# Optimization experiments

Hardware: AMD Instinct MI355X
Metric: run time of the kernel (lower is better)

The kernel has to match this reference:

```python
import jax, jax.numpy as jnp
import numpy as np

# ---- config (mirrors init_kwargs) ----
D_MODEL = 1024
D_STATE = 128
EXPAND = 2
HEADDIM = 64
D_INNER = D_MODEL * EXPAND            # 2048
NHEADS = D_INNER // HEADDIM           # 32
ROPE_FRACTION = 0.5
ROTATE_DIM = (int(D_STATE * ROPE_FRACTION) // 2) * 2   # 64
NUM_ANGLES = ROTATE_DIM // 2          # 32
A_FLOOR = 1e-4
EPS = 1e-5
IN_PROJ_DIM = 2 * D_INNER + 2 * D_STATE + 3 * NHEADS + NUM_ANGLES  # 4480
BATCH, SEQLEN = 2, 2048


def _state_rmsnorm(x, w):
    rms = jnp.sqrt(jnp.mean(x * x, axis=-1, keepdims=True) + EPS)
    return x / rms * w


def _apply_rotary_pairs(x, phase):
    # x: (b,s,h,d_state), phase: (b,s,h,num_pairs)
    if ROTATE_DIM == 0:
        return x
    x_rot = x[..., :ROTATE_DIM].reshape(*x.shape[:-1], ROTATE_DIM // 2, 2)
    x_pass = x[..., ROTATE_DIM:]
    cos = jnp.cos(phase)
    sin = jnp.sin(phase)
    real = x_rot[..., 0]
    imag = x_rot[..., 1]
    rr = real * cos - imag * sin
    ri = real * sin + imag * cos
    rotated = jnp.stack([rr, ri], axis=-1).reshape(*x.shape[:-1], ROTATE_DIM)
    if x_pass.shape[-1] == 0:
        return rotated
    return jnp.concatenate([rotated, x_pass], axis=-1)


def setup_inputs() -> dict:
    key = jax.random.key(0)
    ks = jax.random.split(key, 5)
    x = jax.random.normal(ks[0], (BATCH, SEQLEN, D_MODEL), jnp.float32)
    W_in = jax.random.normal(ks[1], (IN_PROJ_DIM, D_MODEL), jnp.float32) / np.sqrt(D_MODEL)
    # dt_bias ~ inverse-softplus of dt sampled in [dt_min, dt_max]
    dt = jnp.exp(jax.random.uniform(ks[2], (NHEADS,), jnp.float32) * (np.log(0.1) - np.log(0.001)) + np.log(0.001))
    dt = jnp.clip(dt, 1e-4)
    dt_bias = dt + jnp.log(-jnp.expm1(-dt))
    B_norm_w = jnp.ones((D_STATE,), jnp.float32)
    C_norm_w = jnp.ones((D_STATE,), jnp.float32)
    B_bias = jnp.ones((NHEADS, D_STATE), jnp.float32)
    C_bias = jnp.ones((NHEADS, D_STATE), jnp.float32)
    D_param = jnp.ones((NHEADS,), jnp.float32)
    out_norm_w = jnp.ones((D_INNER,), jnp.float32)
    W_out = jax.random.normal(ks[3], (D_MODEL, D_INNER), jnp.float32) / np.sqrt(D_INNER)
    return {"x": x, "W_in": W_in, "dt_bias": dt_bias, "B_norm_w": B_norm_w,
            "C_norm_w": C_norm_w, "B_bias": B_bias, "C_bias": C_bias,
            "D_param": D_param, "out_norm_w": out_norm_w, "W_out": W_out}


def reference(x, W_in, dt_bias, B_norm_w, C_norm_w, B_bias, C_bias, D_param, out_norm_w, W_out):
    b, s, _ = x.shape
    proj = jnp.einsum('bsd,pd->bsp', x, W_in)
    sizes = [D_INNER, D_INNER, D_STATE, D_STATE, NHEADS, NHEADS, NHEADS, NUM_ANGLES]
    offs = np.cumsum([0] + sizes)
    z, v, B_raw, C_raw, dd_dt, dd_A, trap_logits, angle_logits = [
        proj[..., offs[i]:offs[i + 1]] for i in range(8)]
    z = z.reshape(b, s, NHEADS, HEADDIM)
    v = v.reshape(b, s, NHEADS, HEADDIM)
    Bm = _state_rmsnorm(B_raw, B_norm_w)[:, :, None, :] + B_bias[None, None]   # (b,s,h,n)
    Cm = _state_rmsnorm(C_raw, C_norm_w)[:, :, None, :] + C_bias[None, None]
    dt = jax.nn.softplus(dd_dt + dt_bias[None, None])          # (b,s,h)
    A = jnp.minimum(-jax.nn.softplus(dd_A), -A_FLOOR)          # (b,s,h)
    trap = jax.nn.sigmoid(trap_logits)                          # (b,s,h)
    phase = jnp.cumsum(angle_logits, axis=1)[:, :, None, :]     # (b,s,1,angles)
    phase = jnp.broadcast_to(phase, (b, s, NHEADS, NUM_ANGLES))
    Bm = _apply_rotary_pairs(Bm, phase)
    Cm = _apply_rotary_pairs(Cm, phase)

    alpha = jnp.exp(A * dt)               # (b,s,h)
    beta = (1.0 - trap) * dt * alpha
    gamma = trap * dt

    # move time to leading for scan: (s, b, h, ...)
    def tl(a):
        return jnp.moveaxis(a, 1, 0)
    xs = (tl(alpha), tl(beta), tl(gamma), tl(Bm), tl(Cm), tl(v))

    state0 = jnp.zeros((b, NHEADS, HEADDIM, D_STATE), jnp.float32)
    pk0 = jnp.zeros((b, NHEADS, D_STATE), jnp.float32)
    pv0 = jnp.zeros((b, NHEADS, HEADDIM), jnp.float32)

    def step(carry, inp):
        state, pk, pv = carry
        a_t, b_t, g_t, k_t, q_t, v_t = inp
        prev_outer = pv[..., :, None] * pk[..., None, :]        # (b,h,p,n)
        curr_outer = v_t[..., :, None] * k_t[..., None, :]
        state = (a_t[..., None, None] * state
                 + b_t[..., None, None] * prev_outer
                 + g_t[..., None, None] * curr_outer)
        y_t = jnp.einsum('bhpn,bhn->bhp', state, q_t) + D_param[None, :, None] * v_t
        return (state, k_t, v_t), y_t

    _, ys = jax.lax.scan(step, (state0, pk0, pv0), xs)
    y = jnp.moveaxis(ys, 0, 1).reshape(b, s, D_INNER)
    z = z.reshape(b, s, D_INNER)
    # GatedRMSNorm
    rms = jnp.sqrt(jnp.mean(y * y, axis=-1, keepdims=True) + EPS)
    y = (y / rms * out_norm_w) * jax.nn.silu(z)
    return jnp.einsum('bsi,di->bsd', y, W_out)
```

## Files before the change

kernel.cpp:

```cpp
#include <hip/hip_runtime.h>
#include <math.h>

#define S_LEN 2048
#define NBATCH 2
#define DMODEL 1024
#define PDIM 4480
#define DI 2048
#define NH 32
#define HD 64
#define DS 128
#define NA 32
#define CHK 64
#define NC (S_LEN / CHK)
#define OFF_Z 0
#define OFF_V 2048
#define OFF_B 4096
#define OFF_C 4224
#define OFF_DT 4352
#define OFF_A 4384
#define OFF_TRAP 4416
#define OFF_ANG 4448

typedef __attribute__((ext_vector_type(8))) short s8v;
typedef __attribute__((ext_vector_type(4))) float f4v;

__device__ __forceinline__ float softplus_f(float x) {
    return x > 20.f ? x : log1pf(expf(x));
}

__device__ __forceinline__ ushort f2bf(float f) {
    unsigned u = __float_as_uint(f);
    unsigned r = (u + 0x7fffu + ((u >> 16) & 1u)) >> 16;
    return (ushort)r;
}

__device__ __forceinline__ uint4 pack8(const float* f) {
    uint4 o;
    o.x = (unsigned)f2bf(f[0]) | ((unsigned)f2bf(f[1]) << 16);
    o.y = (unsigned)f2bf(f[2]) | ((unsigned)f2bf(f[3]) << 16);
    o.z = (unsigned)f2bf(f[4]) | ((unsigned)f2bf(f[5]) << 16);
    o.w = (unsigned)f2bf(f[6]) | ((unsigned)f2bf(f[7]) << 16);
    return o;
}

__device__ __forceinline__ float bf2f(ushort u) {
    return __uint_as_float(((unsigned)u) << 16);
}
__device__ __forceinline__ float bf_lo(unsigned u) { return __uint_as_float(u << 16); }
__device__ __forceinline__ float bf_hi(unsigned u) { return __uint_as_float(u & 0xffff0000u); }

#define NCX  524288
#define NCWI 573440
#define NCWO 262144
__global__ __launch_bounds__(256)
void f2bf_all(const float* __restrict__ x, const float* __restrict__ wi,
              const float* __restrict__ wo, ushort* __restrict__ xbf,
              ushort* __restrict__ wibf, ushort* __restrict__ wobf) {
    int idx = blockIdx.x * 256 + threadIdx.x;
    const float* src; ushort* dst; int shift, rel;
    if (idx < NCX)              { rel = idx;               src = x;  dst = xbf;  shift = 7; }
    else if (idx < NCX + NCWI)  { rel = idx - NCX;         src = wi; dst = wibf; shift = 7; }
    else                        { rel = idx - NCX - NCWI;  src = wo; dst = wobf; shift = 8; }
    int dc = rel ^ ((rel >> shift) & 7);
    const float* ip = src + (size_t)rel * 8;
    float4 v0 = *(const float4*)ip;
    float4 v1 = *(const float4*)(ip + 4);
    uint4 o;
    o.x = (unsigned)f2bf(v0.x) | ((unsigned)f2bf(v0.y) << 16);
    o.y = (unsigned)f2bf(v0.z) | ((unsigned)f2bf(v0.w) << 16);
    o.z = (unsigned)f2bf(v1.x) | ((unsigned)f2bf(v1.y) << 16);
    o.w = (unsigned)f2bf(v1.z) | ((unsigned)f2bf(v1.w) << 16);
    *(uint4*)(dst + (size_t)dc * 8) = o;
}

__global__ __launch_bounds__(256, 2)
void gemm_bf16(const ushort* __restrict__ A, const ushort* __restrict__ B,
               float* __restrict__ C, int M, int N, int K) {
    __shared__ __align__(16) short lA[128 * 64];
    __shared__ __align__(16) short lB[128 * 64];
    int nwg = gridDim.x;
    int bid = blockIdx.x;
    int q = nwg >> 3;
    int swz = (bid & 7) * q + (bid >> 3);
    int nb = N >> 7;
    int bx = swz % nb, by = swz / nb;

    int tid = threadIdx.x;
    int wv = tid >> 6, ln = tid & 63;
    int rl = ln & 15, kg = ln >> 4, r7 = rl & 7;
    int R0 = (wv >> 1) * 64, C0 = (wv & 1) * 64;

    const ushort* Ag = A + (size_t)(by * 128 + wv * 32 + (ln >> 3)) * K + (ln & 7) * 8;
    const ushort* Bg = B + (size_t)(bx * 128 + wv * 32 + (ln >> 3)) * K + (ln & 7) * 8;
    short* lAw = lA + (wv * 32) * 64;
    short* lBw = lB + (wv * 32) * 64;

    f4v acc[4][4];
#pragma unroll
    for (int m = 0; m < 4; ++m)
#pragma unroll
        for (int n = 0; n < 4; ++n) acc[m][n] = f4v{0.f, 0.f, 0.f, 0.f};

    for (int k0 = 0; k0 < K; k0 += 64) {
        __syncthreads();
#pragma unroll
        for (int i = 0; i < 4; ++i) {
            __builtin_amdgcn_global_load_lds(
                (const __attribute__((address_space(1))) void*)(Ag + (size_t)i * 8 * K + k0),
                (__attribute__((address_space(3))) void*)(lAw + i * 8 * 64), 16, 0, 0);
            __builtin_amdgcn_global_load_lds(
                (const __attribute__((address_space(1))) void*)(Bg + (size_t)i * 8 * K + k0),
                (__attribute__((address_space(3))) void*)(lBw + i * 8 * 64), 16, 0, 0);
        }
        __syncthreads();
#pragma unroll
        for (int ks = 0; ks < 2; ++ks) {
            int kc = ks * 4 + kg;
            int co = ((kc ^ r7) << 3);
            s8v av[4], bv[4];
#pragma unroll
            for (int m = 0; m < 4; ++m)
                av[m] = *(const s8v*)&lA[(R0 + m * 16 + rl) * 64 + co];
#pragma unroll
            for (int n = 0; n < 4; ++n)
                bv[n] = *(const s8v*)&lB[(C0 + n * 16 + rl) * 64 + co];
#pragma unroll
            for (int m = 0; m < 4; ++m)
#pragma unroll
                for (int n = 0; n < 4; ++n)
                    acc[m][n] = __builtin_amdgcn_mfma_f32_16x16x32_bf16(
                        av[m], bv[n], acc[m][n], 0, 0, 0);
        }
    }
#pragma unroll
    for (int m = 0; m < 4; ++m)
#pragma unroll
        for (int n = 0; n < 4; ++n) {
            size_t row0 = (size_t)(by * 128 + R0 + m * 16 + kg * 4);
            int col = bx * 128 + C0 + n * 16 + rl;
#pragma unroll
            for (int r = 0; r < 4; ++r)
                C[(row0 + r) * N + col] = acc[m][n][r];
        }
}

__global__ __launch_bounds__(256)
void phase_kernel(const float* __restrict__ proj, float* __restrict__ cosb,
                  float* __restrict__ sinb) {
    int b = blockIdx.x >> 5;
    int j = blockIdx.x & 31;
    int tid = threadIdx.x;
    __shared__ float part[256];
    float v[8];
    float run = 0.f;
#pragma unroll
    for (int e = 0; e < 8; ++e) {
        int s = tid * 8 + e;
        v[e] = proj[((size_t)(b * S_LEN + s)) * PDIM + OFF_ANG + j];
        run += v[e];
    }
    part[tid] = run;
    __syncthreads();
    for (int off = 1; off < 256; off <<= 1) {
        float add = (tid >= off) ? part[tid - off] : 0.f;
        __syncthreads();
        part[tid] += add;
        __syncthreads();
    }
    float acc = (tid > 0) ? part[tid - 1] : 0.f;
#pragma unroll
    for (int e = 0; e < 8; ++e) {
        acc += v[e];
        int s = tid * 8 + e;
        size_t o = ((size_t)(b * S_LEN + s)) * NA + j;
        cosb[o] = cosf(acc);
        sinb[o] = sinf(acc);
    }
}

__global__ __launch_bounds__(128)
void prep_kernel(const float* __restrict__ proj, const float* __restrict__ dt_bias,
                 const float* __restrict__ Bw, const float* __restrict__ Cw,
                 const float* __restrict__ cosb, const float* __restrict__ sinb,
                 float* __restrict__ Bn, float* __restrict__ Cn,
                 float* __restrict__ ldb, float* __restrict__ wbuf,
                 float* __restrict__ pubuf) {
    size_t row = blockIdx.x;
    int b = (int)(row >> 11);
    int s = (int)(row & 2047);
    int n = threadIdx.x;
    const float* pr = proj + row * PDIM;
    float vB = pr[OFF_B + n];
    float vC = pr[OFF_C + n];
    float sB = vB * vB, sC = vC * vC;
#pragma unroll
    for (int off = 32; off >= 1; off >>= 1) {
        sB += __shfl_xor(sB, off);
        sC += __shfl_xor(sC, off);
    }
    __shared__ float redB[2], redC[2];
    if ((n & 63) == 0) { redB[n >> 6] = sB; redC[n >> 6] = sC; }
    __syncthreads();
    float rB = sqrtf((redB[0] + redB[1]) * (1.f / 128.f) + 1e-5f);
    float rC = sqrtf((redC[0] + redC[1]) * (1.f / 128.f) + 1e-5f);
    float bn = vB / rB * Bw[n];
    float cn = vC / rC * Cw[n];
    float bp = __shfl_xor(bn, 1);
    float cp = __shfl_xor(cn, 1);
    float ob = bn, oc = cn;
    if (n < 64) {
        float c = cosb[row * NA + (n >> 1)];
        float sn_ = sinb[row * NA + (n >> 1)];
        if ((n & 1) == 0) { ob = bn * c - bp * sn_; oc = cn * c - cp * sn_; }
        else              { ob = bp * sn_ + bn * c; oc = cp * sn_ + cn * c; }
    }
    Bn[row * DS + n] = ob;
    Cn[row * DS + n] = oc;
    if (n < NH) {
        int h = n;
        float dtv = softplus_f(pr[OFF_DT + h] + dt_bias[h]);
        float Av = -fmaxf(softplus_f(pr[OFF_A + h]), 1e-4f);
        float trap = 1.f / (1.f + expf(-pr[OFF_TRAP + h]));
        size_t o = ((size_t)(b * NH + h)) * S_LEN + s;
        ldb[o]   = Av * dtv;
        wbuf[o]  = trap * dtv;
        pubuf[o] = (1.f - trap) * dtv;
    }
}

__global__ __launch_bounds__(256)
void lcum_kernel(float* __restrict__ ell) {
    size_t row = blockIdx.x;
    int tid = threadIdx.x;
    float* p = ell + row * S_LEN;
    float v[8];
    float run = 0.f;
#pragma unroll
    for (int e = 0; e < 8; ++e) { v[e] = p[tid * 8 + e]; run += v[e]; }
    __shared__ float part[256];
    part[tid] = run;
    __syncthreads();
    for (int off = 1; off < 256; off <<= 1) {
        float add = (tid >= off) ? part[tid - off] : 0.f;
        __syncthreads();
        part[tid] += add;
        __syncthreads();
    }
    float acc = (tid > 0) ? part[tid - 1] : 0.f;
#pragma unroll
    for (int e = 0; e < 8; ++e) { acc += v[e]; p[tid * 8 + e] = acc; }
}

__device__ __forceinline__ void build32v(
    float* vals, const float* __restrict__ br, const float* __restrict__ bias,
    const float* __restrict__ cr, const float* __restrict__ sr, int rot) {
    float bv[32], bi[32];
#pragma unroll
    for (int j = 0; j < 8; ++j) *(float4*)&bv[j * 4] = *(const float4*)(br + j * 4);
#pragma unroll
    for (int j = 0; j < 8; ++j) *(float4*)&bi[j * 4] = *(const float4*)(bias + j * 4);
    if (rot) {
        float cf[16], sf[16];
#pragma unroll
        for (int j = 0; j < 4; ++j) {
            *(float4*)&cf[j * 4] = *(const float4*)(cr + j * 4);
            *(float4*)&sf[j * 4] = *(const float4*)(sr + j * 4);
        }
#pragma unroll
        for (int a = 0; a < 16; ++a) {
            float c = cf[a], s = sf[a], e = bi[2 * a], o = bi[2 * a + 1];
            vals[2 * a]     = bv[2 * a]     + e * c - o * s;
            vals[2 * a + 1] = bv[2 * a + 1] + e * s + o * c;
        }
    } else {
#pragma unroll
        for (int j = 0; j < 32; ++j) vals[j] = bv[j] + bi[j];
    }
}

__global__ __launch_bounds__(256, 3)
void delta_kernel(const float* __restrict__ proj, const float* __restrict__ Bn,
                  const float* __restrict__ cosb, const float* __restrict__ sinb,
                  const float* __restrict__ ell, const float* __restrict__ wbuf,
                  const float* __restrict__ pubuf, const float* __restrict__ B_bias,
                  ushort* __restrict__ dstate, float* __restrict__ rbuf) {
    __shared__ __align__(16) ushort KT[DS * CHK];
    __shared__ __align__(16) ushort cVT[HD * CHK];
    int blk = blockIdx.x;
    int c = blk & (NC - 1);
    int h = (blk >> 5) & (NH - 1);
    int b = blk >> 10;
    int tid = threadIdx.x;
    size_t row0 = (size_t)b * S_LEN + c * CHK;
    size_t bh = (size_t)b * NH + h;
    int i = tid >> 2, q4 = tid & 3;

    size_t so = bh * S_LEN + c * CHK + i;
    float llast = ell[bh * S_LEN + c * CHK + CHK - 1];
    float li = ell[so];
    float u = wbuf[so];
    if (c * CHK + i < S_LEN - 1) u += pubuf[so + 1];
    float coef = expf(llast - li) * u;
    if (tid == 0) {
        float base = (c == 0) ? 0.f : ell[bh * S_LEN + c * CHK - 1];
        rbuf[blk] = expf(llast - base);
    }
    {
        int n0 = q4 * 32;
        float vals[32];
        build32v(vals, Bn + (row0 + i) * DS + n0, B_bias + h * DS + n0,
                 cosb + (row0 + i) * NA + q4 * 16, sinb + (row0 + i) * NA + q4 * 16,
                 q4 < 2);
#pragma unroll
        for (int j = 0; j < 32; ++j) {
            int n = n0 + j;
            KT[n * 64 + (((i >> 3) ^ (n & 7)) << 3) + (i & 7)] = f2bf(vals[j]);
        }
    }
    {
        int p0 = q4 * 16;
        float vr[16];
        const float* vp = proj + (row0 + i) * PDIM + OFF_V + h * HD + p0;
#pragma unroll
        for (int j = 0; j < 4; ++j) *(float4*)&vr[j * 4] = *(const float4*)(vp + j * 4);
#pragma unroll
        for (int j = 0; j < 16; ++j) {
            int p = p0 + j;
            cVT[p * 64 + (((i >> 3) ^ (p & 7)) << 3) + (i & 7)] = f2bf(vr[j] * coef);
        }
    }
    __syncthreads();
    int wv = tid >> 6, ln = tid & 63, rl = ln & 15, kg = ln >> 4;
    int pA = wv * 16 + rl;
    s8v aV[2];
#pragma unroll
    for (int ks = 0; ks < 2; ++ks)
        aV[ks] = *(const s8v*)&cVT[pA * 64 + (((ks * 4 + kg) ^ (pA & 7)) << 3)];
    ushort* dp = dstate + (size_t)blk * (HD * DS);
#pragma unroll
    for (int nt = 0; nt < 8; ++nt) {
        int nB = nt * 16 + rl;
        f4v dacc = f4v{0.f, 0.f, 0.f, 0.f};
#pragma unroll
        for (int ks = 0; ks < 2; ++ks) {
            s8v bK = *(const s8v*)&KT[nB * 64 + (((ks * 4 + kg) ^ (nB & 7)) << 3)];
            dacc = __builtin_amdgcn_mfma_f32_16x16x32_bf16(aV[ks], bK, dacc, 0, 0, 0);
        }
#pragma unroll
        for (int r = 0; r < 4; ++r) {
            int p = wv * 16 + kg * 4 + r;
            int n = nt * 16 + rl;
            dp[p * DS + (((n >> 3) ^ (p & 7)) << 3) + (n & 7)] = f2bf(dacc[r]);
        }
    }
}

__global__ __launch_bounds__(256)
void state_prop(ushort* __restrict__ dstate, const float* __restrict__ rbuf) {
    size_t bh = blockIdx.x;
    int tid = threadIdx.x;
    float st[32];
#pragma unroll
    for (int j = 0; j < 32; ++j) st[j] = 0.f;
    uint4* base = (uint4*)dstate;
    size_t b0 = bh * NC * 1024ull;
    uint4 nxt[4];
#pragma unroll
    for (int j = 0; j < 4; ++j) nxt[j] = base[b0 + tid * 4 + j];
    for (int c = 0; c < NC; ++c) {
        uint4 cur[4];
#pragma unroll
        for (int j = 0; j < 4; ++j) cur[j] = nxt[j];
        if (c + 1 < NC) {
#pragma unroll
            for (int j = 0; j < 4; ++j)
                nxt[j] = base[b0 + (size_t)(c + 1) * 1024 + tid * 4 + j];
        }
        float r = rbuf[bh * NC + c];
        uint4 outv[4];
#pragma unroll
        for (int j = 0; j < 4; ++j) {
            unsigned uu[4] = {cur[j].x, cur[j].y, cur[j].z, cur[j].w};
            unsigned oo[4];
#pragma unroll
            for (int e = 0; e < 4; ++e) {
                float d0 = bf_lo(uu[e]), d1 = bf_hi(uu[e]);
                int ix = j * 8 + e * 2;
                oo[e] = (unsigned)f2bf(st[ix]) | ((unsigned)f2bf(st[ix + 1]) << 16);
                st[ix]     = fmaf(r, st[ix], d0);
                st[ix + 1] = fmaf(r, st[ix + 1], d1);
            }
            outv[j] = uint4{oo[0], oo[1], oo[2], oo[3]};
        }
#pragma unroll
        for (int j = 0; j < 4; ++j)
            base[b0 + (size_t)c * 1024 + tid * 4 + j] = outv[j];
    }
}

__global__ __launch_bounds__(256, 3)
void out_kernel(const float* __restrict__ proj, const float* __restrict__ Bn,
                const float* __restrict__ Cn, const float* __restrict__ cosb,
                const float* __restrict__ sinb, const float* __restrict__ ell,
                const float* __restrict__ wbuf, const float* __restrict__ pubuf,
                const float* __restrict__ B_bias, const float* __restrict__ C_bias,
                const float* __restrict__ D_param, const ushort* __restrict__ dstate,
                float* __restrict__ y) {
    __shared__ __align__(16) ushort Qb[CHK * DS];
    __shared__ __align__(16) ushort Kb[CHK * DS];
    __shared__ __align__(16) ushort VTb[HD * CHK];
    __shared__ __align__(16) ushort PTb[CHK * CHK];
    __shared__ float s_et[CHK], s_fs[CHK], s_w[CHK];
    int blk = blockIdx.x;
    int c = blk & (NC - 1);
    int h = (blk >> 5) & (NH - 1);
    int b = blk >> 10;
    int tid = threadIdx.x;
    size_t row0 = (size_t)b * S_LEN + c * CHK;
    size_t bh = (size_t)b * NH + h;
    int i = tid >> 2, q4 = tid & 3;

    if (q4 == 0) {
        size_t so = bh * S_LEN + c * CHK + i;
        float base = (c == 0) ? 0.f : ell[bh * S_LEN + c * CHK - 1];
        float lp = ell[so] - base;
        float wv_ = wbuf[so];
        float u = wv_;
        if (c * CHK + i < S_LEN - 1) u += pubuf[so + 1];
        s_et[i] = expf(lp);
        s_fs[i] = u * expf(fminf(-lp, 80.f));
        s_w[i] = wv_;
    }
    {
        int n0 = q4 * 32;
        float vals[32];
        build32v(vals, Cn + (row0 + i) * DS + n0, C_bias + h * DS + n0,
                 cosb + (row0 + i) * NA + q4 * 16, sinb + (row0 + i) * NA + q4 * 16,
                 q4 < 2);
#pragma unroll
        for (int j = 0; j < 4; ++j) {
            int cc = (q4 * 4 + j) ^ (i & 7);
            *(uint4*)&Qb[i * 128 + cc * 8] = pack8(&vals[j * 8]);
        }
    }
    {
        int n0 = q4 * 32;
        float vals[32];
        build32v(vals, Bn + (row0 + i) * DS + n0, B_bias + h * DS + n0,
                 cosb + (row0 + i) * NA + q4 * 16, sinb + (row0 + i) * NA + q4 * 16,
                 q4 < 2);
#pragma unroll
        for (int j = 0; j < 4; ++j) {
            int cc = (q4 * 4 + j) ^ (i & 7);
            *(uint4*)&Kb[i * 128 + cc * 8] = pack8(&vals[j * 8]);
        }
    }
    {
        int p0 = q4 * 16;
        float vr[16];
        const float* vp = proj + (row0 + i) * PDIM + OFF_V + h * HD + p0;
#pragma unroll
        for (int j = 0; j < 4; ++j) *(float4*)&vr[j * 4] = *(const float4*)(vp + j * 4);
#pragma unroll
        for (int j = 0; j < 16; ++j) {
            int p = p0 + j;
            VTb[p * 64 + (((i >> 3) ^ (p & 7)) << 3) + (i & 7)] = f2bf(vr[j]);
        }
    }
    __syncthreads();

    int wv2 = tid >> 6, ln = tid & 63, rl = ln & 15, kg = ln >> 4;
    int tA = wv2 * 16 + rl;
    s8v aQ[4];
#pragma unroll
    for (int kc = 0; kc < 4; ++kc)
        aQ[kc] = *(const s8v*)&Qb[tA * 128 + (((kc * 4 + kg) ^ (tA & 7)) << 3)];
    f4v pacc[4];
#pragma unroll
    for (int st = 0; st < 4; ++st) pacc[st] = f4v{0.f, 0.f, 0.f, 0.f};
#pragma unroll
    for (int st = 0; st < 4; ++st) {
        int sB = st * 16 + rl;
#pragma unroll
        for (int kc = 0; kc < 4; ++kc) {
            s8v bK = *(const s8v*)&Kb[sB * 128 + (((kc * 4 + kg) ^ (sB & 7)) << 3)];
            pacc[st] = __builtin_amdgcn_mfma_f32_16x16x32_bf16(aQ[kc], bK, pacc[st], 0, 0, 0);
        }
    }
    __syncthreads();

    {
        const ushort* sg = dstate + (size_t)blk * (CHK * DS);
#pragma unroll
        for (int k = 0; k < 4; ++k) {
            int ch = wv2 * 256 + k * 64;
            __builtin_amdgcn_global_load_lds(
                (const __attribute__((address_space(1))) void*)(sg + (size_t)(ch + ln) * 8),
                (__attribute__((address_space(3))) void*)(Kb + ch * 8), 16, 0, 0);
        }
    }
#pragma unroll
    for (int st = 0; st < 4; ++st) {
        int s = st * 16 + rl;
#pragma unroll
        for (int r = 0; r < 4; ++r) {
            int t2 = wv2 * 16 + kg * 4 + r;
            float m;
            if (s < t2)       m = s_et[t2] * s_fs[s];
            else if (s == t2) m = s_w[t2];
            else              m = 0.f;
            PTb[t2 * 64 + (((s >> 3) ^ (t2 & 7)) << 3) + (s & 7)] = f2bf(pacc[st][r] * m);
        }
    }
    __syncthreads();

    s8v aP[2];
#pragma unroll
    for (int ks = 0; ks < 2; ++ks)
        aP[ks] = *(const s8v*)&PTb[tA * 64 + (((ks * 4 + kg) ^ (tA & 7)) << 3)];
    f4v y1[4], y2[4];
#pragma unroll
    for (int pt = 0; pt < 4; ++pt) { y1[pt] = f4v{0.f,0.f,0.f,0.f}; y2[pt] = f4v{0.f,0.f,0.f,0.f}; }
#pragma unroll
    for (int pt = 0; pt < 4; ++pt) {
        int pB = pt * 16 + rl;
#pragma unroll
        for (int ks = 0; ks < 2; ++ks) {
            s8v bV = *(const s8v*)&VTb[pB * 64 + (((ks * 4 + kg) ^ (pB & 7)) << 3)];
            y1[pt] = __builtin_amdgcn_mfma_f32_16x16x32_bf16(aP[ks], bV, y1[pt], 0, 0, 0);
        }
#pragma unroll
        for (int kc = 0; kc < 4; ++kc) {
            s8v bS = *(const s8v*)&Kb[pB * 128 + (((kc * 4 + kg) ^ (pB & 7)) << 3)];
            y2[pt] = __builtin_amdgcn_mfma_f32_16x16x32_bf16(aQ[kc], bS, y2[pt], 0, 0, 0);
        }
    }
    float Dp = D_param[h];
#pragma unroll
    for (int pt = 0; pt < 4; ++pt) {
#pragma unroll
        for (int r = 0; r < 4; ++r) {
            int t2 = wv2 * 16 + kg * 4 + r;
            int p = pt * 16 + rl;
            float v = bf2f(VTb[p * 64 + (((t2 >> 3) ^ (p & 7)) << 3) + (t2 & 7)]);
            y[(row0 + t2) * DI + h * HD + p] = y1[pt][r] + s_et[t2] * y2[pt][r] + Dp * v;
        }
    }
}

__global__ __launch_bounds__(256)
void ynorm_kernel(const float* __restrict__ y, const float* __restrict__ proj,
                  const float* __restrict__ w, ushort* __restrict__ ybf) {
    size_t row = blockIdx.x;
    int tid = threadIdx.x;
    const float* yr = y + row * (size_t)DI;
    float4 v0 = *(const float4*)(yr + tid * 8);
    float4 v1 = *(const float4*)(yr + tid * 8 + 4);
    float ss = v0.x * v0.x + v0.y * v0.y + v0.z * v0.z + v0.w * v0.w +
               v1.x * v1.x + v1.y * v1.y + v1.z * v1.z + v1.w * v1.w;
#pragma unroll
    for (int off = 32; off >= 1; off >>= 1) ss += __shfl_xor(ss, off);
    __shared__ float red[4];
    if ((tid & 63) == 0) red[tid >> 6] = ss;
    __syncthreads();
    float tot = red[0] + red[1] + red[2] + red[3];
    float rinv = 1.f / sqrtf(tot * (1.f / 2048.f) + 1e-5f);
    const float* zr = proj + row * (size_t)PDIM + OFF_Z;
    float4 z0 = *(const float4*)(zr + tid * 8);
    float4 z1 = *(const float4*)(zr + tid * 8 + 4);
    float4 w0 = *(const float4*)(w + tid * 8);
    float4 w1 = *(const float4*)(w + tid * 8 + 4);
    float yv[8] = {v0.x, v0.y, v0.z, v0.w, v1.x, v1.y, v1.z, v1.w};
    float zv[8] = {z0.x, z0.y, z0.z, z0.w, z1.x, z1.y, z1.z, z1.w};
    float wv[8] = {w0.x, w0.y, w0.z, w0.w, w1.x, w1.y, w1.z, w1.w};
    ushort u[8];
#pragma unroll
    for (int e = 0; e < 8; ++e) {
        float sil = zv[e] / (1.f + expf(-zv[e]));
        u[e] = f2bf(yv[e] * rinv * wv[e] * sil);
    }
    int dstc = (tid & ~7) | ((tid & 7) ^ ((int)row & 7));
    uint4 o;
    o.x = (unsigned)u[0] | ((unsigned)u[1] << 16);
    o.y = (unsigned)u[2] | ((unsigned)u[3] << 16);
    o.z = (unsigned)u[4] | ((unsigned)u[5] << 16);
    o.w = (unsigned)u[6] | ((unsigned)u[7] << 16);
    *(uint4*)(ybf + row * (size_t)DI + dstc * 8) = o;
}

extern "C" void kernel_launch(void* const* d_in, const int* in_sizes, int n_in,
                              void* d_out, int out_size, void* d_ws, size_t ws_size,
                              hipStream_t stream) {
    const float* x          = (const float*)d_in[0];
    const float* W_in       = (const float*)d_in[1];
    const float* dt_bias    = (const float*)d_in[2];
    const float* B_norm_w   = (const float*)d_in[3];
    const float* C_norm_w   = (const float*)d_in[4];
    const float* B_bias     = (const float*)d_in[5];
    const float* C_bias     = (const float*)d_in[6];
    const float* D_param    = (const float*)d_in[7];
    const float* out_norm_w = (const float*)d_in[8];
    const float* W_out      = (const float*)d_in[9];
    float* out = (float*)d_out;

    const size_t M = (size_t)NBATCH * S_LEN;
    const size_t NBLK = (size_t)NBATCH * NH * NC;
    float* ws = (float*)d_ws;
    size_t off = 0;
    float* proj  = ws + off; off += M * PDIM;
    float* cosb  = ws + off; off += M * NA;
    float* sinb  = ws + off; off += M * NA;
    float* Bn    = ws + off; off += M * DS;
    float* Cn    = ws + off; off += M * DS;
    float* ell   = ws + off; off += (size_t)NBATCH * NH * S_LEN;
    float* wbuf  = ws + off; off += (size_t)NBATCH * NH * S_LEN;
    float* pubuf = ws + off; off += (size_t)NBATCH * NH * S_LEN;
    float* y     = ws + off; off += M * DI;
    float* rbuf  = ws + off; off += NBLK;
    ushort* xbf  = (ushort*)(ws + off); off += M * DMODEL / 2;
    ushort* wibf = (ushort*)(ws + off); off += (size_t)PDIM * DMODEL / 2;
    ushort* wobf = (ushort*)(ws + off); off += (size_t)DMODEL * DI / 2;
    ushort* ybf  = (ushort*)(ws + off); off += M * DI / 2;
    ushort* dstate = (ushort*)(ws + off); off += NBLK * CHK * DS / 2;

    f2bf_all<<<dim3((NCX + NCWI + NCWO) / 256), 256, 0, stream>>>(
        x, W_in, W_out, xbf, wibf, wobf);
    gemm_bf16<<<dim3((PDIM / 128) * (int)(M / 128)), 256, 0, stream>>>(xbf, wibf, proj, (int)M, PDIM, DMODEL);
    phase_kernel<<<dim3(NBATCH * NA), 256, 0, stream>>>(proj, cosb, sinb);
    prep_kernel<<<dim3((int)M), 128, 0, stream>>>(proj, dt_bias, B_norm_w, C_norm_w,
                                                  cosb, sinb, Bn, Cn, ell, wbuf, pubuf);
    lcum_kernel<<<dim3(NBATCH * NH), 256, 0, stream>>>(ell);
    delta_kernel<<<dim3((int)NBLK), 256, 0, stream>>>(proj, Bn, cosb, sinb, ell,
                                                      wbuf, pubuf, B_bias, dstate, rbuf);
    state_prop<<<dim3(NBATCH * NH), 256, 0, stream>>>(dstate, rbuf);
    out_kernel<<<dim3((int)NBLK), 256, 0, stream>>>(proj, Bn, Cn, cosb, sinb, ell,
                                                    wbuf, pubuf, B_bias, C_bias,
                                                    D_param, dstate, y);
    ynorm_kernel<<<dim3((int)M), 256, 0, stream>>>(y, proj, out_norm_w, ybf);
    gemm_bf16<<<dim3((DMODEL / 128) * (int)(M / 128)), 256, 0, stream>>>(ybf, wobf, out, (int)M, DMODEL, DI);
}
```

Baseline: 252.6 us.

## Reuse bf16 V tiles across kernels and move D skip term into ynorm

The delta kernel now also writes a bf16, pre-swizzled transposed V tile per chunk to a workspace buffer. The output kernel loads that tile straight into LDS with global_load_lds instead of re-reading and converting fp32 V from the projection. The output kernel writes y in a chunk-blocked layout without the D·v term, and ynorm gathers from that layout and adds D·v. Launch-bound occupancy hints rise for the GEMM and delta kernels, which may force register spills; the change also adds an extra workspace buffer and gathered reads in ynorm.

```diff
diff --git a/kernel.cpp b/kernel.cpp
--- a/kernel.cpp
+++ b/kernel.cpp
@@ -73,7 +73,7 @@
     *(uint4*)(dst + (size_t)dc * 8) = o;
 }
 
-__global__ __launch_bounds__(256, 2)
+__global__ __launch_bounds__(256, 4)
 void gemm_bf16(const ushort* __restrict__ A, const ushort* __restrict__ B,
                float* __restrict__ C, int M, int N, int K) {
     __shared__ __align__(16) short lA[128 * 64];
@@ -278,14 +278,16 @@
     }
 }
 
-__global__ __launch_bounds__(256, 3)
+__global__ __launch_bounds__(256, 4)
 void delta_kernel(const float* __restrict__ proj, const float* __restrict__ Bn,
                   const float* __restrict__ cosb, const float* __restrict__ sinb,
                   const float* __restrict__ ell, const float* __restrict__ wbuf,
                   const float* __restrict__ pubuf, const float* __restrict__ B_bias,
-                  ushort* __restrict__ dstate, float* __restrict__ rbuf) {
+                  ushort* __restrict__ dstate, ushort* __restrict__ vtbuf,
+                  float* __restrict__ rbuf) {
     __shared__ __align__(16) ushort KT[DS * CHK];
     __shared__ __align__(16) ushort cVT[HD * CHK];
+    __shared__ __align__(16) ushort VT[HD * CHK];
     int blk = blockIdx.x;
     int c = blk & (NC - 1);
     int h = (blk >> 5) & (NH - 1);
@@ -326,10 +328,18 @@
 #pragma unroll
         for (int j = 0; j < 16; ++j) {
             int p = p0 + j;
-            cVT[p * 64 + (((i >> 3) ^ (p & 7)) << 3) + (i & 7)] = f2bf(vr[j] * coef);
-        }
-    }
-    __syncthreads();
+            int addr = p * 64 + (((i >> 3) ^ (p & 7)) << 3) + (i & 7);
+            VT[addr]  = f2bf(vr[j]);
+            cVT[addr] = f2bf(vr[j] * coef);
+        }
+    }
+    __syncthreads();
+    {
+        const uint4* vs = (const uint4*)VT;
+        uint4* vd = (uint4*)(vtbuf + (size_t)blk * (HD * CHK));
+        vd[tid] = vs[tid];
+        vd[tid + 256] = vs[tid + 256];
+    }
     int wv = tid >> 6, ln = tid & 63, rl = ln & 15, kg = ln >> 4;
     int pA = wv * 16 + rl;
     s8v aV[2];
@@ -399,13 +409,12 @@
 }
 
 __global__ __launch_bounds__(256, 3)
-void out_kernel(const float* __restrict__ proj, const float* __restrict__ Bn,
-                const float* __restrict__ Cn, const float* __restrict__ cosb,
-                const float* __restrict__ sinb, const float* __restrict__ ell,
-                const float* __restrict__ wbuf, const float* __restrict__ pubuf,
-                const float* __restrict__ B_bias, const float* __restrict__ C_bias,
-                const float* __restrict__ D_param, const ushort* __restrict__ dstate,
-                float* __restrict__ y) {
+void out_kernel(const float* __restrict__ Bn, const float* __restrict__ Cn,
+                const float* __restrict__ cosb, const float* __restrict__ sinb,
+                const float* __restrict__ ell, const float* __restrict__ wbuf,
+                const float* __restrict__ pubuf, const float* __restrict__ B_bias,
+                const float* __restrict__ C_bias, const ushort* __restrict__ dstate,
+                const ushort* __restrict__ vtbuf, float* __restrict__ yb) {
     __shared__ __align__(16) ushort Qb[CHK * DS];
     __shared__ __align__(16) ushort Kb[CHK * DS];
     __shared__ __align__(16) ushort VTb[HD * CHK];
@@ -419,7 +428,18 @@
     size_t row0 = (size_t)b * S_LEN + c * CHK;
     size_t bh = (size_t)b * NH + h;
     int i = tid >> 2, q4 = tid & 3;
-
+    int wv2 = tid >> 6, ln = tid & 63;
+
+    {
+        const ushort* vg = vtbuf + (size_t)blk * (HD * CHK);
+#pragma unroll
+        for (int k = 0; k < 2; ++k) {
+            int ch = wv2 * 128 + k * 64;
+            __builtin_amdgcn_global_load_lds(
+                (const __attribute__((address_space(1))) void*)(vg + (size_t)(ch + ln) * 8),
+                (__attribute__((address_space(3))) void*)(VTb + ch * 8), 16, 0, 0);
+        }
+    }
     if (q4 == 0) {
         size_t so = bh * S_LEN + c * CHK + i;
         float base = (c == 0) ? 0.f : ell[bh * S_LEN + c * CHK - 1];
@@ -455,21 +475,9 @@
             *(uint4*)&Kb[i * 128 + cc * 8] = pack8(&vals[j * 8]);
         }
     }
-    {
-        int p0 = q4 * 16;
-        float vr[16];
-        const float* vp = proj + (row0 + i) * PDIM + OFF_V + h * HD + p0;
-#pragma unroll
-        for (int j = 0; j < 4; ++j) *(float4*)&vr[j * 4] = *(const float4*)(vp + j * 4);
-#pragma unroll
-        for (int j = 0; j < 16; ++j) {
-            int p = p0 + j;
-            VTb[p * 64 + (((i >> 3) ^ (p & 7)) << 3) + (i & 7)] = f2bf(vr[j]);
-        }
-    }
-    __syncthreads();
-
-    int wv2 = tid >> 6, ln = tid & 63, rl = ln & 15, kg = ln >> 4;
+    __syncthreads();
+
+    int rl = ln & 15, kg = ln >> 4;
     int tA = wv2 * 16 + rl;
     s8v aQ[4];
 #pragma unroll
@@ -535,29 +543,41 @@
             y2[pt] = __builtin_amdgcn_mfma_f32_16x16x32_bf16(aQ[kc], bS, y2[pt], 0, 0, 0);
         }
     }
-    float Dp = D_param[h];
+    float* yp = yb + (size_t)blk * (CHK * HD);
 #pragma unroll
     for (int pt = 0; pt < 4; ++pt) {
 #pragma unroll
         for (int r = 0; r < 4; ++r) {
             int t2 = wv2 * 16 + kg * 4 + r;
             int p = pt * 16 + rl;
-            float v = bf2f(VTb[p * 64 + (((t2 >> 3) ^ (p & 7)) << 3) + (t2 & 7)]);
-            y[(row0 + t2) * DI + h * HD + p] = y1[pt][r] + s_et[t2] * y2[pt][r] + Dp * v;
+            yp[t2 * HD + p] = y1[pt][r] + s_et[t2] * y2[pt][r];
         }
     }
 }
 
 __global__ __launch_bounds__(256)
-void ynorm_kernel(const float* __restrict__ y, const float* __restrict__ proj,
-                  const float* __restrict__ w, ushort* __restrict__ ybf) {
+void ynorm_kernel(const float* __restrict__ yb, const float* __restrict__ proj,
+                  const float* __restrict__ w, const float* __restrict__ D_param,
+                  ushort* __restrict__ ybf) {
     size_t row = blockIdx.x;
+    int b = (int)(row >> 11);
+    int s = (int)(row & 2047);
+    int c = s >> 6, t = s & 63;
     int tid = threadIdx.x;
-    const float* yr = y + row * (size_t)DI;
-    float4 v0 = *(const float4*)(yr + tid * 8);
-    float4 v1 = *(const float4*)(yr + tid * 8 + 4);
-    float ss = v0.x * v0.x + v0.y * v0.y + v0.z * v0.z + v0.w * v0.w +
-               v1.x * v1.x + v1.y * v1.y + v1.z * v1.z + v1.w * v1.w;
+    int hh = tid >> 3;
+    int p0 = (tid * 8) & 63;
+    const float* yr = yb + (((size_t)(b * NH + hh) * NC + c) * CHK + t) * HD + p0;
+    float4 v0 = *(const float4*)yr;
+    float4 v1 = *(const float4*)(yr + 4);
+    const float* vr = proj + row * (size_t)PDIM + OFF_V + tid * 8;
+    float4 vv0 = *(const float4*)vr;
+    float4 vv1 = *(const float4*)(vr + 4);
+    float Dp = D_param[hh];
+    float yv[8] = {v0.x + Dp * vv0.x, v0.y + Dp * vv0.y, v0.z + Dp * vv0.z, v0.w + Dp * vv0.w,
+                   v1.x + Dp * vv1.x, v1.y + Dp * vv1.y, v1.z + Dp * vv1.z, v1.w + Dp * vv1.w};
+    float ss = 0.f;
+#pragma unroll
+    for (int e = 0; e < 8; ++e) ss += yv[e] * yv[e];
 #pragma unroll
     for (int off = 32; off >= 1; off >>= 1) ss += __shfl_xor(ss, off);
     __shared__ float red[4];
@@ -570,7 +590,6 @@
     float4 z1 = *(const float4*)(zr + tid * 8 + 4);
     float4 w0 = *(const float4*)(w + tid * 8);
     float4 w1 = *(const float4*)(w + tid * 8 + 4);
-    float yv[8] = {v0.x, v0.y, v0.z, v0.w, v1.x, v1.y, v1.z, v1.w};
     float zv[8] = {z0.x, z0.y, z0.z, z0.w, z1.x, z1.y, z1.z, z1.w};
     float wv[8] = {w0.x, w0.y, w0.z, w0.w, w1.x, w1.y, w1.z, w1.w};
     ushort u[8];
@@ -615,13 +634,14 @@
     float* ell   = ws + off; off += (size_t)NBATCH * NH * S_LEN;
     float* wbuf  = ws + off; off += (size_t)NBATCH * NH * S_LEN;
     float* pubuf = ws + off; off += (size_t)NBATCH * NH * S_LEN;
-    float* y     = ws + off; off += M * DI;
+    float* yb    = ws + off; off += NBLK * CHK * HD;
     float* rbuf  = ws + off; off += NBLK;
     ushort* xbf  = (ushort*)(ws + off); off += M * DMODEL / 2;
     ushort* wibf = (ushort*)(ws + off); off += (size_t)PDIM * DMODEL / 2;
     ushort* wobf = (ushort*)(ws + off); off += (size_t)DMODEL * DI / 2;
     ushort* ybf  = (ushort*)(ws + off); off += M * DI / 2;
     ushort* dstate = (ushort*)(ws + off); off += NBLK * CHK * DS / 2;
+    ushort* vtbuf  = (ushort*)(ws + off); off += NBLK * HD * CHK / 2;
 
     f2bf_all<<<dim3((NCX + NCWI + NCWO) / 256), 256, 0, stream>>>(
         x, W_in, W_out, xbf, wibf, wobf);
@@ -631,11 +651,12 @@
                                                   cosb, sinb, Bn, Cn, ell, wbuf, pubuf);
     lcum_kernel<<<dim3(NBATCH * NH), 256, 0, stream>>>(ell);
     delta_kernel<<<dim3((int)NBLK), 256, 0, stream>>>(proj, Bn, cosb, sinb, ell,
-                                                      wbuf, pubuf, B_bias, dstate, rbuf);
+                                                      wbuf, pubuf, B_bias, dstate,
+                                                      vtbuf, rbuf);
     state_prop<<<dim3(NBATCH * NH), 256, 0, stream>>>(dstate, rbuf);
-    out_kernel<<<dim3((int)NBLK), 256, 0, stream>>>(proj, Bn, Cn, cosb, sinb, ell,
+    out_kernel<<<dim3((int)NBLK), 256, 0, stream>>>(Bn, Cn, cosb, sinb, ell,
                                                     wbuf, pubuf, B_bias, C_bias,
-                                                    D_param, dstate, y);
-    ynorm_kernel<<<dim3((int)M), 256, 0, stream>>>(y, proj, out_norm_w, ybf);
+                                                    dstate, vtbuf, yb);
+    ynorm_kernel<<<dim3((int)M), 256, 0, stream>>>(yb, proj, out_norm_w, D_param, ybf);
     gemm_bf16<<<dim3((DMODEL / 128) * (int)(M / 128)), 256, 0, stream>>>(ybf, wobf, out, (int)M, DMODEL, DI);
 }
```

After: 256.6 us. No clear change (+1.6%).
